# Kernel tuning notes

Hardware: AMD Instinct MI355X
Metric: run time of the kernel (lower is better)

Reference implementation:

```python
import jax, jax.numpy as jnp
import numpy as np

K = 7            # involution kernel size
GC = 16          # group_channels (hardcoded in module)
EPS = 1e-5       # BatchNorm eps


def setup_inputs() -> dict:
    key = jax.random.key(0)
    ks = jax.random.split(key, 5)
    C, R = 256, 4
    mid = C // R                      # 64
    groups = C // GC                  # 16
    B, H, W = 4, 56, 56
    x = jax.random.normal(ks[0], (B, C, H, W), dtype=jnp.float32)
    w1 = jax.random.normal(ks[1], (mid, C), dtype=jnp.float32) * (1.0 / np.sqrt(C))
    b1 = jax.random.normal(ks[2], (mid,), dtype=jnp.float32) * 0.01
    gamma = jnp.ones((mid,), dtype=jnp.float32)
    beta = jnp.zeros((mid,), dtype=jnp.float32)
    w2 = jax.random.normal(ks[3], (K * K * groups, mid), dtype=jnp.float32) * (1.0 / np.sqrt(mid))
    b2 = jax.random.normal(ks[4], (K * K * groups,), dtype=jnp.float32) * 0.01
    return {"x": x, "w1": w1, "b1": b1, "gamma": gamma, "beta": beta, "w2": w2, "b2": b2}


def reference(x, w1, b1, gamma, beta, w2, b2):
    B, C, H, W = x.shape
    groups = C // GC
    k2 = K * K
    pad = (K - 1) // 2

    # weight branch: 1x1 conv -> BN (batch stats, training-mode math) -> ReLU -> 1x1 conv
    t = jnp.einsum('oc,bchw->bohw', w1, x) + b1[None, :, None, None]
    mu = t.mean(axis=(0, 2, 3), keepdims=True)
    var = ((t - mu) ** 2).mean(axis=(0, 2, 3), keepdims=True)
    t = (t - mu) * jax.lax.rsqrt(var + EPS)
    t = t * gamma[None, :, None, None] + beta[None, :, None, None]
    t = jax.nn.relu(t)
    wgt = jnp.einsum('ot,bthw->bohw', w2, t) + b2[None, :, None, None]
    wgt = wgt.reshape(B, groups, k2, H, W)              # per-pixel kernels

    # unfold: kernel positions row-major (i over kh, j over kw), channel-major layout
    xp = jnp.pad(x, ((0, 0), (0, 0), (pad, pad), (pad, pad)))
    patches = jnp.stack(
        [xp[:, :, i:i + H, j:j + W] for i in range(K) for j in range(K)], axis=2
    )                                                   # [B, C, k2, H, W]
    patches = patches.reshape(B, groups, GC, k2, H, W)

    out = jnp.einsum('bgkhw,bgckhw->bgchw', wgt, patches)  # weighted sum over k2
    return out.reshape(B, C, H, W)
```

## Files before the change

kernel.cpp:

```cpp
#include <hip/hip_runtime.h>
#include <hip/hip_bf16.h>

typedef short bf16x8 __attribute__((ext_vector_type(8)));
typedef float f32x4  __attribute__((ext_vector_type(4)));

#define KSZ   7
#define KK    49
#define GCH   16
#define CIN   256
#define MID   64
#define NGRP  16
#define WID   56
#define HWSZ  3136
#define NB    4
#define NPIX  (NB * HWSZ)
#define EPSV  1e-5f

#define WS_W1T 256
#define WS_T   (256 + CIN * MID)

__global__ __launch_bounds__(256) void k0_transpose(const float* __restrict__ w1,
                                                    float* __restrict__ ws) {
    const int i = blockIdx.x * 256 + threadIdx.x;
    const int c = i >> 6;
    const int o = i & 63;
    ws[WS_W1T + i] = w1[o * CIN + c];
}

__global__ __launch_bounds__(256) void k1_conv1(const float* __restrict__ x,
                                                const float* __restrict__ b1,
                                                float* __restrict__ ws) {
    const int tid = threadIdx.x;
    const int pix = blockIdx.x * 256 + tid;
    const int ob  = blockIdx.y * 4;
    const int b   = pix / HWSZ;
    const int hw  = pix - b * HWSZ;

    float acc[4];
#pragma unroll
    for (int i = 0; i < 4; ++i) acc[i] = b1[ob + i];

    const float* xp = x + (size_t)b * CIN * HWSZ + hw;
    const float* wT = ws + WS_W1T + ob;
#pragma unroll 16
    for (int c = 0; c < CIN; ++c) {
        const float4 wv = *(const float4*)(wT + c * MID);
        const float  xv = xp[(size_t)c * HWSZ];
        acc[0] = fmaf(wv.x, xv, acc[0]);
        acc[1] = fmaf(wv.y, xv, acc[1]);
        acc[2] = fmaf(wv.z, xv, acc[2]);
        acc[3] = fmaf(wv.w, xv, acc[3]);
    }

    float* tp = ws + WS_T + (size_t)ob * NPIX + pix;
#pragma unroll
    for (int i = 0; i < 4; ++i) tp[(size_t)i * NPIX] = acc[i];

    __shared__ float bs[4];
    __shared__ float bq[4];
    if (tid < 4) { bs[tid] = 0.f; bq[tid] = 0.f; }
    __syncthreads();
#pragma unroll
    for (int i = 0; i < 4; ++i) {
        float s = acc[i];
        float qq = acc[i] * acc[i];
#pragma unroll
        for (int m = 1; m < 64; m <<= 1) {
            s  += __shfl_xor(s, m, 64);
            qq += __shfl_xor(qq, m, 64);
        }
        if ((tid & 63) == 0) { atomicAdd(&bs[i], s); atomicAdd(&bq[i], qq); }
    }
    __syncthreads();
    if (tid < 4) {
        atomicAdd(&ws[ob + tid],      bs[tid]);
        atomicAdd(&ws[64 + ob + tid], bq[tid]);
    }
}

__global__ void k2_stats(float* __restrict__ ws,
                         const float* __restrict__ gamma,
                         const float* __restrict__ beta) {
    const int o = threadIdx.x;
    const float n   = (float)NPIX;
    const float mu  = ws[o] / n;
    const float var = ws[64 + o] / n - mu * mu;
    const float a   = gamma[o] * rsqrtf(var + EPSV);
    ws[128 + o] = a;
    ws[192 + o] = beta[o] - mu * a;
}

__global__ __launch_bounds__(512) void k3_fused(const float* __restrict__ x,
                                                const float* __restrict__ w2,
                                                const float* __restrict__ b2,
                                                const float* __restrict__ ws,
                                                float* __restrict__ out) {
    __shared__ unsigned short tlb[128][72];
    __shared__ unsigned short wb[64][72];
    __shared__ float swgt[128][52];
    const int tid  = threadIdx.x;
    const int p    = tid & 127;
    const int q    = tid >> 7;
    const int lane = tid & 63;
    const int wave = tid >> 6;
    const int g    = blockIdx.y;
    const int pix  = blockIdx.x * 128 + p;

    {
        const float* tcol = ws + WS_T + blockIdx.x * 128 + p;
        bf16x8 v0, v1;
#pragma unroll
        for (int i = 0; i < 16; ++i) {
            const int o = q * 16 + i;
            float v = tcol[(size_t)o * NPIX];
            v = fmaxf(0.f, fmaf(ws[128 + o], v, ws[192 + o]));
            __hip_bfloat16 hb = __float2bfloat16(v);
            const short s = *reinterpret_cast<short*>(&hb);
            if (i < 8) v0[i & 7] = s; else v1[i & 7] = s;
        }
        *(bf16x8*)&tlb[p][q * 16]     = v0;
        *(bf16x8*)&tlb[p][q * 16 + 8] = v1;
    }

    for (int e = tid; e < 64 * 64; e += 512) {
        const int row = e >> 6;
        const int k   = e & 63;
        const float v = (row < KK) ? w2[((size_t)g * KK + row) * MID + k] : 0.f;
        __hip_bfloat16 hb = __float2bfloat16(v);
        wb[row][k] = *reinterpret_cast<unsigned short*>(&hb);
    }
    __syncthreads();

    {
        const int m  = wave >> 1;
        const int n0 = (wave & 1) * 4;
        const int r  = lane & 15;
        const int hi = lane >> 4;
        f32x4 acc[4] = {{0,0,0,0},{0,0,0,0},{0,0,0,0},{0,0,0,0}};
#pragma unroll
        for (int ks = 0; ks < 2; ++ks) {
            const bf16x8 af = *(const bf16x8*)&wb[m * 16 + r][ks * 32 + hi * 8];
#pragma unroll
            for (int ni = 0; ni < 4; ++ni) {
                const bf16x8 bfv = *(const bf16x8*)&tlb[(n0 + ni) * 16 + r][ks * 32 + hi * 8];
                acc[ni] = __builtin_amdgcn_mfma_f32_16x16x32_bf16(af, bfv, acc[ni], 0, 0, 0);
            }
        }
#pragma unroll
        for (int ni = 0; ni < 4; ++ni) {
            const int px = (n0 + ni) * 16 + r;
#pragma unroll
            for (int j = 0; j < 4; ++j) {
                const int tap = m * 16 + hi * 4 + j;
                if (tap < KK) swgt[px][tap] = acc[ni][j];
            }
        }
    }
    __syncthreads();

    const int b  = pix / HWSZ;
    const int hw = pix - b * HWSZ;
    const int h  = hw / WID;
    const int w  = hw - h * WID;
    const float* xq   = x + ((size_t)b * CIN + g * GCH + q * 4) * HWSZ;
    const float* bias = b2 + g * KK;

    float a0 = 0.f, a1 = 0.f, a2 = 0.f, a3 = 0.f;
    bool colok[7];
#pragma unroll
    for (int j = 0; j < 7; ++j) colok[j] = (unsigned)(w + j - 3) < 56u;

#pragma unroll
    for (int r7 = 0; r7 < 7; ++r7) {
        const bool rowok = (unsigned)(h + r7 - 3) < 56u;
        const int  roff  = hw + (r7 - 3) * WID - 3;
#pragma unroll
        for (int j = 0; j < 7; ++j) {
            const int   t   = r7 * 7 + j;
            const float wgv = swgt[p][t] + bias[t];
            const float wm  = (rowok && colok[j]) ? wgv : 0.f;
            int idx = roff + j;
            idx = idx < 0 ? 0 : idx;
            idx = idx > (HWSZ - 1) ? (HWSZ - 1) : idx;
            a0 = fmaf(wm, xq[idx],            a0);
            a1 = fmaf(wm, xq[idx + HWSZ],     a1);
            a2 = fmaf(wm, xq[idx + 2 * HWSZ], a2);
            a3 = fmaf(wm, xq[idx + 3 * HWSZ], a3);
        }
    }

    float* ob = out + ((size_t)b * CIN + g * GCH + q * 4) * HWSZ + hw;
    ob[0]        = a0;
    ob[HWSZ]     = a1;
    ob[2 * HWSZ] = a2;
    ob[3 * HWSZ] = a3;
}

extern "C" void kernel_launch(void* const* d_in, const int* in_sizes, int n_in,
                              void* d_out, int out_size, void* d_ws, size_t ws_size,
                              hipStream_t stream) {
    const float* x     = (const float*)d_in[0];
    const float* w1    = (const float*)d_in[1];
    const float* b1    = (const float*)d_in[2];
    const float* gamma = (const float*)d_in[3];
    const float* beta  = (const float*)d_in[4];
    const float* w2    = (const float*)d_in[5];
    const float* b2    = (const float*)d_in[6];
    float* out = (float*)d_out;
    float* ws  = (float*)d_ws;

    hipMemsetAsync(ws, 0, 128 * sizeof(float), stream);

    k0_transpose<<<dim3(64), 256, 0, stream>>>(w1, ws);
    k1_conv1<<<dim3(49, 16), 256, 0, stream>>>(x, b1, ws);
    k2_stats<<<1, 64, 0, stream>>>(ws, gamma, beta);
    k3_fused<<<dim3(98, 16), 512, 0, stream>>>(x, w2, b2, ws, out);
}
```

Baseline: 101.0 us.

## Rewrite pipeline with MFMA conv1, bf16 intermediates, and channel-interleaved x layout

Replaces the scalar FMA first 1x1 conv with a bf16 MFMA kernel and stores the intermediate activations as bf16 instead of fp32. The BN-stats kernel is folded into the final kernel's prologue, and w1/w2 are pre-converted to bf16 in a single packing kernel. When the workspace is large enough, x is also repacked into a group-interleaved layout so the involution can read four channels with one float4 load per tap. The final kernel moves to 64-pixel, 256-thread blocks with aliased shared memory. In exchange, the first conv and the stored intermediates now run in reduced precision, and the repack adds an extra full pass over x.

```diff
diff --git a/kernel.cpp b/kernel.cpp
--- a/kernel.cpp
+++ b/kernel.cpp
@@ -4,7 +4,6 @@
 typedef short bf16x8 __attribute__((ext_vector_type(8)));
 typedef float f32x4  __attribute__((ext_vector_type(4)));
 
-#define KSZ   7
 #define KK    49
 #define GCH   16
 #define CIN   256
@@ -13,163 +12,217 @@
 #define WID   56
 #define HWSZ  3136
 #define NB    4
-#define NPIX  (NB * HWSZ)
+#define NPIX  12544
 #define EPSV  1e-5f
 
-#define WS_W1T 256
-#define WS_T   (256 + CIN * MID)
-
-__global__ __launch_bounds__(256) void k0_transpose(const float* __restrict__ w1,
-                                                    float* __restrict__ ws) {
-    const int i = blockIdx.x * 256 + threadIdx.x;
-    const int c = i >> 6;
-    const int o = i & 63;
-    ws[WS_W1T + i] = w1[o * CIN + c];
-}
-
-__global__ __launch_bounds__(256) void k1_conv1(const float* __restrict__ x,
+#define WS_SUM   0
+#define WS_W1BF  128
+#define WS_W2BF  8320
+#define WS_T     41088
+#define WS_XI    442496
+#define WS_XI_END 3653760
+
+__device__ inline unsigned short f2bf(float f) {
+    __hip_bfloat16 h = __float2bfloat16(f);
+    return *reinterpret_cast<unsigned short*>(&h);
+}
+__device__ inline float bf2f(unsigned short s) {
+    return __uint_as_float(((unsigned)s) << 16);
+}
+__device__ inline unsigned pack2(float lo, float hi) {
+    return ((unsigned)f2bf(hi) << 16) | (unsigned)f2bf(lo);
+}
+
+__global__ __launch_bounds__(256) void kA_pack(const float* __restrict__ x,
+                                               const float* __restrict__ w1,
+                                               const float* __restrict__ w2,
+                                               float* __restrict__ ws) {
+    const int bid = blockIdx.x;
+    if (bid < 64) {
+        const int i = bid * 256 + threadIdx.x;
+        ((unsigned short*)(ws + WS_W1BF))[i] = f2bf(w1[i]);
+    } else if (bid < 320) {
+        const int i = (bid - 64) * 256 + threadIdx.x;
+        const int g = i >> 12, row = (i >> 6) & 63, k = i & 63;
+        const float v = (row < KK) ? w2[((size_t)(g * KK + row)) * MID + k] : 0.f;
+        ((unsigned short*)(ws + WS_W2BF))[i] = f2bf(v);
+    } else {
+        const int pg = (bid - 320) * 256 + threadIdx.x;
+        const int b   = pg / (NGRP * HWSZ);
+        const int rem = pg - b * NGRP * HWSZ;
+        const int g   = rem / HWSZ;
+        const int hw  = rem - g * HWSZ;
+        const float* xs = x + ((size_t)(b * CIN + g * GCH)) * HWSZ + hw;
+        float v[16];
+#pragma unroll
+        for (int i = 0; i < 16; ++i) v[i] = xs[(size_t)i * HWSZ];
+        float4* dst = (float4*)(ws + WS_XI + (size_t)pg * 16);
+        dst[0] = make_float4(v[0], v[1], v[2], v[3]);
+        dst[1] = make_float4(v[4], v[5], v[6], v[7]);
+        dst[2] = make_float4(v[8], v[9], v[10], v[11]);
+        dst[3] = make_float4(v[12], v[13], v[14], v[15]);
+    }
+}
+
+__global__ __launch_bounds__(256) void kB_conv1(const float* __restrict__ x,
                                                 const float* __restrict__ b1,
                                                 float* __restrict__ ws) {
-    const int tid = threadIdx.x;
-    const int pix = blockIdx.x * 256 + tid;
-    const int ob  = blockIdx.y * 4;
-    const int b   = pix / HWSZ;
-    const int hw  = pix - b * HWSZ;
-
-    float acc[4];
-#pragma unroll
-    for (int i = 0; i < 4; ++i) acc[i] = b1[ob + i];
-
-    const float* xp = x + (size_t)b * CIN * HWSZ + hw;
-    const float* wT = ws + WS_W1T + ob;
-#pragma unroll 16
-    for (int c = 0; c < CIN; ++c) {
-        const float4 wv = *(const float4*)(wT + c * MID);
-        const float  xv = xp[(size_t)c * HWSZ];
-        acc[0] = fmaf(wv.x, xv, acc[0]);
-        acc[1] = fmaf(wv.y, xv, acc[1]);
-        acc[2] = fmaf(wv.z, xv, acc[2]);
-        acc[3] = fmaf(wv.w, xv, acc[3]);
-    }
-
-    float* tp = ws + WS_T + (size_t)ob * NPIX + pix;
-#pragma unroll
-    for (int i = 0; i < 4; ++i) tp[(size_t)i * NPIX] = acc[i];
-
-    __shared__ float bs[4];
-    __shared__ float bq[4];
-    if (tid < 4) { bs[tid] = 0.f; bq[tid] = 0.f; }
-    __syncthreads();
-#pragma unroll
-    for (int i = 0; i < 4; ++i) {
-        float s = acc[i];
-        float qq = acc[i] * acc[i];
-#pragma unroll
-        for (int m = 1; m < 64; m <<= 1) {
+    __shared__ unsigned short xtb[64][266];
+    __shared__ unsigned short w1b[64][266];
+    const int tid  = threadIdx.x;
+    const int lane = tid & 63, r = lane & 15, hi = lane >> 4;
+    const int wave = tid >> 6;
+    const int pix0 = blockIdx.x * 64;
+    const int b    = pix0 / HWSZ;
+    const int hw0  = pix0 - b * HWSZ;
+
+    {
+        const unsigned short* w1bf = (const unsigned short*)(ws + WS_W1BF);
+#pragma unroll
+        for (int e = tid; e < 2048; e += 256) {
+            const int row = e >> 5, c8 = (e & 31) * 8;
+            *(bf16x8*)&w1b[row][c8] = *(const bf16x8*)(w1bf + row * 256 + c8);
+        }
+    }
+    {
+        const int px = tid & 63;
+        const int ks = tid >> 6;
+        const float* xs = x + (size_t)b * CIN * HWSZ + hw0 + px;
+#pragma unroll
+        for (int pass = 0; pass < 8; ++pass) {
+            const int k0 = pass * 32 + ks * 8;
+            unsigned pk[4];
+#pragma unroll
+            for (int u = 0; u < 4; ++u)
+                pk[u] = pack2(xs[(size_t)(k0 + 2 * u) * HWSZ],
+                              xs[(size_t)(k0 + 2 * u + 1) * HWSZ]);
+            *(bf16x8*)&xtb[px][k0] = *(bf16x8*)pk;
+        }
+    }
+    __syncthreads();
+
+    const float4 bv = *(const float4*)(b1 + wave * 16 + hi * 4);
+    f32x4 acc[4];
+#pragma unroll
+    for (int ni = 0; ni < 4; ++ni) { acc[ni][0]=bv.x; acc[ni][1]=bv.y; acc[ni][2]=bv.z; acc[ni][3]=bv.w; }
+#pragma unroll
+    for (int ks = 0; ks < 8; ++ks) {
+        const bf16x8 af = *(const bf16x8*)&w1b[wave * 16 + r][ks * 32 + hi * 8];
+#pragma unroll
+        for (int ni = 0; ni < 4; ++ni) {
+            const bf16x8 bfv = *(const bf16x8*)&xtb[ni * 16 + r][ks * 32 + hi * 8];
+            acc[ni] = __builtin_amdgcn_mfma_f32_16x16x32_bf16(af, bfv, acc[ni], 0, 0, 0);
+        }
+    }
+
+    unsigned short* tws = (unsigned short*)(ws + WS_T);
+#pragma unroll
+    for (int j = 0; j < 4; ++j) {
+        const int mid = wave * 16 + hi * 4 + j;
+        float s = 0.f, qq = 0.f;
+#pragma unroll
+        for (int ni = 0; ni < 4; ++ni) {
+            const float v = acc[ni][j];
+            tws[(size_t)mid * NPIX + pix0 + ni * 16 + r] = f2bf(v);
+            s += v; qq += v * v;
+        }
+#pragma unroll
+        for (int m = 1; m < 16; m <<= 1) {
             s  += __shfl_xor(s, m, 64);
             qq += __shfl_xor(qq, m, 64);
         }
-        if ((tid & 63) == 0) { atomicAdd(&bs[i], s); atomicAdd(&bq[i], qq); }
-    }
-    __syncthreads();
-    if (tid < 4) {
-        atomicAdd(&ws[ob + tid],      bs[tid]);
-        atomicAdd(&ws[64 + ob + tid], bq[tid]);
-    }
-}
-
-__global__ void k2_stats(float* __restrict__ ws,
-                         const float* __restrict__ gamma,
-                         const float* __restrict__ beta) {
-    const int o = threadIdx.x;
-    const float n   = (float)NPIX;
-    const float mu  = ws[o] / n;
-    const float var = ws[64 + o] / n - mu * mu;
-    const float a   = gamma[o] * rsqrtf(var + EPSV);
-    ws[128 + o] = a;
-    ws[192 + o] = beta[o] - mu * a;
-}
-
-__global__ __launch_bounds__(512) void k3_fused(const float* __restrict__ x,
-                                                const float* __restrict__ w2,
+        if (r == 0) {
+            atomicAdd(&ws[WS_SUM + mid],      s);
+            atomicAdd(&ws[WS_SUM + 64 + mid], qq);
+        }
+    }
+}
+
+template <int USE_XI>
+__global__ __launch_bounds__(256) void kC_fused(const float* __restrict__ x,
                                                 const float* __restrict__ b2,
+                                                const float* __restrict__ gamma,
+                                                const float* __restrict__ beta,
                                                 const float* __restrict__ ws,
                                                 float* __restrict__ out) {
-    __shared__ unsigned short tlb[128][72];
-    __shared__ unsigned short wb[64][72];
-    __shared__ float swgt[128][52];
+    __shared__ char lbuf[18944];
+    __shared__ float a_s[64], c_s[64];
+    unsigned short (*tlb)[74] = (unsigned short(*)[74])lbuf;
+    unsigned short (*wb)[74]  = (unsigned short(*)[74])(lbuf + 9472);
+    float (*swgt)[53]         = (float(*)[53])lbuf;
+
     const int tid  = threadIdx.x;
-    const int p    = tid & 127;
-    const int q    = tid >> 7;
-    const int lane = tid & 63;
+    const int lane = tid & 63, r = lane & 15, hi = lane >> 4;
     const int wave = tid >> 6;
+    const int q    = __builtin_amdgcn_readfirstlane(wave);
+    const int px   = tid & 63;
+    const int pix0 = blockIdx.x * 64;
     const int g    = blockIdx.y;
-    const int pix  = blockIdx.x * 128 + p;
-
-    {
-        const float* tcol = ws + WS_T + blockIdx.x * 128 + p;
-        bf16x8 v0, v1;
-#pragma unroll
-        for (int i = 0; i < 16; ++i) {
-            const int o = q * 16 + i;
-            float v = tcol[(size_t)o * NPIX];
-            v = fmaxf(0.f, fmaf(ws[128 + o], v, ws[192 + o]));
-            __hip_bfloat16 hb = __float2bfloat16(v);
-            const short s = *reinterpret_cast<short*>(&hb);
-            if (i < 8) v0[i & 7] = s; else v1[i & 7] = s;
-        }
-        *(bf16x8*)&tlb[p][q * 16]     = v0;
-        *(bf16x8*)&tlb[p][q * 16 + 8] = v1;
-    }
-
-    for (int e = tid; e < 64 * 64; e += 512) {
-        const int row = e >> 6;
-        const int k   = e & 63;
-        const float v = (row < KK) ? w2[((size_t)g * KK + row) * MID + k] : 0.f;
-        __hip_bfloat16 hb = __float2bfloat16(v);
-        wb[row][k] = *reinterpret_cast<unsigned short*>(&hb);
-    }
-    __syncthreads();
-
-    {
-        const int m  = wave >> 1;
-        const int n0 = (wave & 1) * 4;
-        const int r  = lane & 15;
-        const int hi = lane >> 4;
-        f32x4 acc[4] = {{0,0,0,0},{0,0,0,0},{0,0,0,0},{0,0,0,0}};
-#pragma unroll
-        for (int ks = 0; ks < 2; ++ks) {
-            const bf16x8 af = *(const bf16x8*)&wb[m * 16 + r][ks * 32 + hi * 8];
-#pragma unroll
-            for (int ni = 0; ni < 4; ++ni) {
-                const bf16x8 bfv = *(const bf16x8*)&tlb[(n0 + ni) * 16 + r][ks * 32 + hi * 8];
-                acc[ni] = __builtin_amdgcn_mfma_f32_16x16x32_bf16(af, bfv, acc[ni], 0, 0, 0);
-            }
-        }
+    const int b    = pix0 / HWSZ;
+    const int hw0  = pix0 - b * HWSZ;
+
+    if (tid < 64) {
+        const float n   = (float)NPIX;
+        const float mu  = ws[WS_SUM + tid] / n;
+        const float var = ws[WS_SUM + 64 + tid] / n - mu * mu;
+        const float a   = gamma[tid] * rsqrtf(var + EPSV);
+        a_s[tid] = a;
+        c_s[tid] = beta[tid] - mu * a;
+    }
+    __syncthreads();
+
+    {
+        const unsigned short* tws = (const unsigned short*)(ws + WS_T);
+        unsigned pk[8];
+#pragma unroll
+        for (int u = 0; u < 8; ++u) {
+            const int k = q * 16 + 2 * u;
+            float v0 = bf2f(tws[(size_t)k * NPIX + pix0 + px]);
+            float v1 = bf2f(tws[(size_t)(k + 1) * NPIX + pix0 + px]);
+            v0 = fmaxf(0.f, fmaf(a_s[k], v0, c_s[k]));
+            v1 = fmaxf(0.f, fmaf(a_s[k + 1], v1, c_s[k + 1]));
+            pk[u] = pack2(v0, v1);
+        }
+        *(bf16x8*)&tlb[px][q * 16]     = *(bf16x8*)&pk[0];
+        *(bf16x8*)&tlb[px][q * 16 + 8] = *(bf16x8*)&pk[4];
+    }
+    {
+        const unsigned short* src = (const unsigned short*)(ws + WS_W2BF) + (size_t)g * 4096;
+#pragma unroll
+        for (int e = tid; e < 512; e += 256) {
+            const int row = e >> 3, c8 = (e & 7) * 8;
+            *(bf16x8*)&wb[row][c8] = *(const bf16x8*)(src + row * 64 + c8);
+        }
+    }
+    __syncthreads();
+
+    f32x4 acc[4] = {{0,0,0,0},{0,0,0,0},{0,0,0,0},{0,0,0,0}};
+#pragma unroll
+    for (int ks = 0; ks < 2; ++ks) {
+        const bf16x8 af = *(const bf16x8*)&wb[wave * 16 + r][ks * 32 + hi * 8];
 #pragma unroll
         for (int ni = 0; ni < 4; ++ni) {
-            const int px = (n0 + ni) * 16 + r;
-#pragma unroll
-            for (int j = 0; j < 4; ++j) {
-                const int tap = m * 16 + hi * 4 + j;
-                if (tap < KK) swgt[px][tap] = acc[ni][j];
-            }
-        }
-    }
-    __syncthreads();
-
-    const int b  = pix / HWSZ;
-    const int hw = pix - b * HWSZ;
-    const int h  = hw / WID;
-    const int w  = hw - h * WID;
-    const float* xq   = x + ((size_t)b * CIN + g * GCH + q * 4) * HWSZ;
-    const float* bias = b2 + g * KK;
-
+            const bf16x8 bfv = *(const bf16x8*)&tlb[ni * 16 + r][ks * 32 + hi * 8];
+            acc[ni] = __builtin_amdgcn_mfma_f32_16x16x32_bf16(af, bfv, acc[ni], 0, 0, 0);
+        }
+    }
+    __syncthreads();
+#pragma unroll
+    for (int ni = 0; ni < 4; ++ni)
+#pragma unroll
+        for (int j = 0; j < 4; ++j) {
+            const int tap = wave * 16 + hi * 4 + j;
+            if (tap < KK) swgt[ni * 16 + r][tap] = acc[ni][j];
+        }
+    __syncthreads();
+
+    const int hw = hw0 + px;
+    const int h  = hw / WID, w = hw - h * WID;
+    const float* b2g = b2 + g * KK;
     float a0 = 0.f, a1 = 0.f, a2 = 0.f, a3 = 0.f;
-    bool colok[7];
-#pragma unroll
-    for (int j = 0; j < 7; ++j) colok[j] = (unsigned)(w + j - 3) < 56u;
-
+
+    const float* xb4 = USE_XI ? (ws + WS_XI + ((size_t)(b * NGRP + g) * HWSZ) * 16 + q * 4)
+                              : (x + ((size_t)(b * CIN + g * GCH + q * 4)) * HWSZ);
 #pragma unroll
     for (int r7 = 0; r7 < 7; ++r7) {
         const bool rowok = (unsigned)(h + r7 - 3) < 56u;
@@ -177,19 +230,27 @@
 #pragma unroll
         for (int j = 0; j < 7; ++j) {
             const int   t   = r7 * 7 + j;
-            const float wgv = swgt[p][t] + bias[t];
-            const float wm  = (rowok && colok[j]) ? wgv : 0.f;
+            const float wgv = swgt[px][t] + b2g[t];
+            const bool  ok  = rowok && ((unsigned)(w + j - 3) < 56u);
+            const float wm  = ok ? wgv : 0.f;
             int idx = roff + j;
-            idx = idx < 0 ? 0 : idx;
-            idx = idx > (HWSZ - 1) ? (HWSZ - 1) : idx;
-            a0 = fmaf(wm, xq[idx],            a0);
-            a1 = fmaf(wm, xq[idx + HWSZ],     a1);
-            a2 = fmaf(wm, xq[idx + 2 * HWSZ], a2);
-            a3 = fmaf(wm, xq[idx + 3 * HWSZ], a3);
-        }
-    }
-
-    float* ob = out + ((size_t)b * CIN + g * GCH + q * 4) * HWSZ + hw;
+            idx = idx < 0 ? 0 : (idx > HWSZ - 1 ? HWSZ - 1 : idx);
+            if (USE_XI) {
+                const float4 xv = *(const float4*)(xb4 + (size_t)idx * 16);
+                a0 = fmaf(wm, xv.x, a0);
+                a1 = fmaf(wm, xv.y, a1);
+                a2 = fmaf(wm, xv.z, a2);
+                a3 = fmaf(wm, xv.w, a3);
+            } else {
+                a0 = fmaf(wm, xb4[idx],            a0);
+                a1 = fmaf(wm, xb4[idx + HWSZ],     a1);
+                a2 = fmaf(wm, xb4[idx + 2 * HWSZ], a2);
+                a3 = fmaf(wm, xb4[idx + 3 * HWSZ], a3);
+            }
+        }
+    }
+
+    float* ob = out + ((size_t)(b * CIN + g * GCH + q * 4)) * HWSZ + hw;
     ob[0]        = a0;
     ob[HWSZ]     = a1;
     ob[2 * HWSZ] = a2;
@@ -209,10 +270,13 @@
     float* out = (float*)d_out;
     float* ws  = (float*)d_ws;
 
+    const bool use_xi = ws_size >= (size_t)WS_XI_END * sizeof(float);
+
     hipMemsetAsync(ws, 0, 128 * sizeof(float), stream);
-
-    k0_transpose<<<dim3(64), 256, 0, stream>>>(w1, ws);
-    k1_conv1<<<dim3(49, 16), 256, 0, stream>>>(x, b1, ws);
-    k2_stats<<<1, 64, 0, stream>>>(ws, gamma, beta);
-    k3_fused<<<dim3(98, 16), 512, 0, stream>>>(x, w2, b2, ws, out);
-}
+    kA_pack<<<use_xi ? 1104 : 320, 256, 0, stream>>>(x, w1, w2, ws);
+    kB_conv1<<<196, 256, 0, stream>>>(x, b1, ws);
+    if (use_xi)
+        kC_fused<1><<<dim3(196, 16), 256, 0, stream>>>(x, b2, gamma, beta, ws, out);
+    else
+        kC_fused<0><<<dim3(196, 16), 256, 0, stream>>>(x, b2, gamma, beta, ws, out);
+}
```

Result: slower. 127.2 us (+25.9%).
